# Kernel optimization log

Measured on AMD Instinct MI355X. Metric: run time of the kernel, lower is better.

The kernel has to match this reference:

```python
import jax, jax.numpy as jnp
import numpy as np

# SMPL kinematic tree (parents[0] is the root and unused in the loop)
PARENTS = (0, 0, 0, 0, 1, 2, 3, 4, 5, 6, 7, 8, 9, 9, 9, 12, 13, 14, 16, 17, 18, 19, 20, 21)
N_BATCH, N_VERTS, N_JOINTS, N_BETAS, N_POSE, N_COCO = 1024, 6890, 24, 10, 207, 19


def setup_inputs() -> dict:
    key = jax.random.key(0)
    ks = jax.random.split(key, 8)
    return {
        "beta": jax.random.normal(ks[0], (N_BATCH, N_BETAS), jnp.float32) * 0.5,
        "theta": jax.random.normal(ks[1], (N_BATCH, N_JOINTS * 3), jnp.float32) * 0.3,
        "v_template": jax.random.normal(ks[2], (N_VERTS, 3), jnp.float32),
        "shapedirs": jax.random.normal(ks[3], (N_BETAS, N_VERTS * 3), jnp.float32) * 0.01,
        "J_regressor": jax.random.uniform(ks[4], (N_VERTS, N_JOINTS), jnp.float32) / N_VERTS,
        "posedirs": jax.random.normal(ks[5], (N_POSE, N_VERTS * 3), jnp.float32) * 0.01,
        "weights": jax.random.uniform(ks[6], (N_VERTS, N_JOINTS), jnp.float32),
        "joint_regressor": jax.random.uniform(ks[7], (N_VERTS, N_COCO), jnp.float32) / N_VERTS,
    }


def batch_rodrigues(theta):
    """theta: (M, 3) axis-angle -> (M, 3, 3) rotation matrices."""
    angle = jnp.sqrt(jnp.sum(theta * theta, axis=-1, keepdims=True) + 1e-8)  # (M,1)
    r = theta / angle
    c = jnp.cos(angle)[..., None]  # (M,1,1)
    s = jnp.sin(angle)[..., None]
    rx, ry, rz = r[:, 0], r[:, 1], r[:, 2]
    z = jnp.zeros_like(rx)
    K = jnp.stack([z, -rz, ry, rz, z, -rx, -ry, rx, z], axis=-1).reshape(-1, 3, 3)
    outer = r[:, :, None] * r[:, None, :]
    eye = jnp.eye(3, dtype=theta.dtype)
    return c * eye + s * K + (1.0 - c) * outer


def global_rigid_transform(Rs, J):
    """Rs: (N,24,3,3), J: (N,24,3) -> (J_transformed (N,24,3), A (N,24,4,4))."""
    N = Rs.shape[0]
    bot = jnp.broadcast_to(jnp.array([0.0, 0.0, 0.0, 1.0], Rs.dtype), (N, 1, 4))

    def make_A(R, t):  # R: (N,3,3), t: (N,3)
        top = jnp.concatenate([R, t[:, :, None]], axis=2)  # (N,3,4)
        return jnp.concatenate([top, bot], axis=1)  # (N,4,4)

    results = [make_A(Rs[:, 0], J[:, 0])]
    for i in range(1, N_JOINTS):
        t_rel = J[:, i] - J[:, PARENTS[i]]
        results.append(jnp.matmul(results[PARENTS[i]], make_A(Rs[:, i], t_rel)))
    res = jnp.stack(results, axis=1)  # (N,24,4,4)
    J_transformed = res[:, :, :3, 3]
    # A = res - pack(res @ [J; 0]) : subtract rotated rest joints from translation column
    J_homo = jnp.concatenate([J, jnp.zeros((N, N_JOINTS, 1), Rs.dtype)], axis=2)  # (N,24,4)
    init_bone = jnp.einsum('njab,njb->nja', res, J_homo)  # (N,24,4)
    A = res - jnp.concatenate([jnp.zeros((N, N_JOINTS, 4, 3), Rs.dtype), init_bone[..., None]], axis=-1)
    return J_transformed, A


def reference(beta, theta, v_template, shapedirs, J_regressor, posedirs, weights, joint_regressor):
    N = beta.shape[0]
    # shape blend: (N,10) @ (10, V*3) -> (N,V,3)
    v_shaped = (beta @ shapedirs).reshape(N, N_VERTS, 3) + v_template
    # rest-pose joints: (N,V,3) x (V,24) -> (N,24,3)
    J = jnp.einsum('nva,vj->nja', v_shaped, J_regressor)
    # pose rotations
    Rs = batch_rodrigues(theta.reshape(-1, 3)).reshape(N, N_JOINTS, 3, 3)
    # pose blend: (N,207) @ (207, V*3)
    pose_feature = (Rs[:, 1:] - jnp.eye(3, dtype=Rs.dtype)).reshape(N, N_POSE)
    v_posed = (pose_feature @ posedirs).reshape(N, N_VERTS, 3) + v_shaped
    # kinematic chain
    _, A = global_rigid_transform(Rs, J)
    # LBS: per-vertex 4x4 transform
    T = jnp.einsum('vj,njab->nvab', weights, A)  # (N,V,4,4)
    v_homo = jnp.concatenate([v_posed, jnp.ones((N, N_VERTS, 1), v_posed.dtype)], axis=2)
    verts = jnp.einsum('nvab,nvb->nva', T, v_homo)[:, :, :3]  # (N,V,3)
    joints = jnp.einsum('nva,vj->nja', verts, joint_regressor)  # (N,19,3)
    return joints
```

## Files before the change

kernel.cpp:

```cpp
#include <hip/hip_runtime.h>

#define NB 1024
#define NV 6890
#define VP 6912
#define NJ 24
#define NBETA 10
#define NPOSE 207
#define NK 19
#define NKJ 456
#define NCOL 1368
#define KR 218
#define AR 219
#define VSTR 20670
#define RTP 16
#define NVC 216
#define CFP 32
#define KSPLIT 12
#define KSTEPS 18

typedef __attribute__((ext_vector_type(8))) short bf16x8;
typedef __attribute__((ext_vector_type(4))) float f32x4;

#define AP_PLANE ((size_t)3*RTP*NVC*64*8)
#define BP_PLANE ((size_t)CFP*NVC*64*8)
#define USH_TOTAL (2*AP_PLANE + 2*BP_PLANE)
#define SZ_OUT   ((size_t)AR*NCOL)
#define SZ_COEF  ((size_t)KR*NB)
#define SZ_AW    ((size_t)NB*288)
#define SZ_JS    (11ull*24*3)
#define SZ_M     ((size_t)NB*NCOL)

__device__ inline void bf_split(float x, unsigned short& h, unsigned short& l) {
    unsigned u = __float_as_uint(x);
    h = (unsigned short)(u >> 16);
    float hf = __uint_as_float((unsigned)h << 16);
    float lf = x - hf;
    l = (unsigned short)(__float_as_uint(lf) >> 16);
}

__global__ __launch_bounds__(256) void k_at2(const float* __restrict__ pd,
                                             const float* __restrict__ sd,
                                             const float* __restrict__ vt,
                                             unsigned short* __restrict__ APH,
                                             unsigned short* __restrict__ APL) {
    int tid = threadIdx.x;
    int u = blockIdx.x * 4 + (tid >> 6);
    int rt = u / NVC, vc = u - rt * NVC;
    int rl = tid & 15, lh = (tid >> 4) & 3;
    int r = rt * 16 + rl;
    int v0 = (vc * 4 + lh) * 8;

    float f[24];
    if (r >= AR) {
#pragma unroll
        for (int i = 0; i < 24; i++) f[i] = 0.f;
    } else if (r == 218) {
#pragma unroll
        for (int i = 0; i < 24; i++) f[i] = (v0 + i / 3 < NV) ? 1.0f : 0.f;
    } else {
        const float* src = (r < NPOSE) ? (pd + (size_t)r * VSTR)
                         : (r < 217)   ? (sd + (size_t)(r - NPOSE) * VSTR)
                                       : vt;
        if (v0 + 8 <= NV) {
            const float2* p = (const float2*)(src + 3 * v0);
#pragma unroll
            for (int q = 0; q < 12; q++) {
                float2 t = p[q];
                f[2 * q] = t.x; f[2 * q + 1] = t.y;
            }
        } else {
#pragma unroll
            for (int i = 0; i < 24; i++)
                f[i] = (v0 + i / 3 < NV) ? src[3 * v0 + i] : 0.f;
        }
    }

    int lane = lh * 16 + rl;
#pragma unroll
    for (int a = 0; a < 3; a++) {
        union { unsigned short u16[8]; int4 v4; } H, L;
#pragma unroll
        for (int e = 0; e < 8; e++) bf_split(f[3 * e + a], H.u16[e], L.u16[e]);
        size_t off = (((size_t)(a * RTP + rt) * NVC + vc) * 64 + lane) * 8;
        *(int4*)&APH[off] = H.v4;
        *(int4*)&APL[off] = L.v4;
    }
}

__global__ __launch_bounds__(256) void k_cw2(const float* __restrict__ jr,
                                             const float* __restrict__ w,
                                             unsigned short* __restrict__ BPH,
                                             unsigned short* __restrict__ BPL) {
    int tid = threadIdx.x;
    int u = blockIdx.x * 4 + (tid >> 6);
    int cf = u / NVC, vc = u - cf * NVC;
    int cl = tid & 15, lh = (tid >> 4) & 3;
    int col = cf * 16 + cl;
    int v0 = (vc * 4 + lh) * 8;
    int k = col / NJ, j = col - k * NJ;
    bool okc = (col < NKJ);

    union { unsigned short u16[8]; int4 v4; } H, L;
#pragma unroll
    for (int e = 0; e < 8; e++) {
        int v = v0 + e;
        float val = (okc && v < NV) ? jr[v * NK + k] * w[v * NJ + j] : 0.f;
        bf_split(val, H.u16[e], L.u16[e]);
    }
    size_t off = (((size_t)cf * NVC + vc) * 64 + (lh * 16 + cl)) * 8;
    *(int4*)&BPH[off] = H.v4;
    *(int4*)&BPL[off] = L.v4;
}

__global__ __launch_bounds__(256) void k_js2(const float* __restrict__ Jreg,
                                             const float* __restrict__ sd,
                                             const float* __restrict__ vt,
                                             float* __restrict__ JS) {
    int row = blockIdx.x % 11;
    int c   = blockIdx.x / 11;
    int tid = threadIdx.x;
    int lane = tid & 63;
    const float* src = (row < NBETA) ? (sd + (size_t)row * VSTR) : vt;

    float acc[72];
#pragma unroll
    for (int o = 0; o < 72; o++) acc[o] = 0.f;

    for (int iv = 0; iv < 4; ++iv) {
        int v = c * 1024 + iv * 256 + tid;
        float jrg[24];
        float s0 = 0.f, s1 = 0.f, s2 = 0.f;
        if (v < NV) {
#pragma unroll
            for (int q = 0; q < 6; q++) {
                float4 f = *(const float4*)&Jreg[v * NJ + q * 4];
                jrg[q * 4 + 0] = f.x; jrg[q * 4 + 1] = f.y;
                jrg[q * 4 + 2] = f.z; jrg[q * 4 + 3] = f.w;
            }
            s0 = src[3 * v]; s1 = src[3 * v + 1]; s2 = src[3 * v + 2];
        } else {
#pragma unroll
            for (int q = 0; q < 24; q++) jrg[q] = 0.f;
        }
#pragma unroll
        for (int j = 0; j < 24; j++) {
            acc[j * 3 + 0] += jrg[j] * s0;
            acc[j * 3 + 1] += jrg[j] * s1;
            acc[j * 3 + 2] += jrg[j] * s2;
        }
    }
#pragma unroll
    for (int o = 0; o < 72; o++) {
#pragma unroll
        for (int off = 1; off < 64; off <<= 1)
            acc[o] += __shfl_xor(acc[o], off);
    }
    if (lane == 0) {
#pragma unroll
        for (int o = 0; o < 72; o++) atomicAdd(&JS[row * 72 + o], acc[o]);
    }
}

__global__ __launch_bounds__(64) void k_pose(const float* __restrict__ beta,
                                             const float* __restrict__ theta,
                                             const float* __restrict__ JS,
                                             float* __restrict__ coefT,
                                             float* __restrict__ Aw) {
    int n = blockIdx.x;
    int tid = threadIdx.x;
    __shared__ float Rs[24][9];
    __shared__ float Jl[24][3];
    __shared__ float G[24][12];

    if (tid < NJ) {
        int j = tid;
        float x = theta[n * 72 + j * 3 + 0];
        float y = theta[n * 72 + j * 3 + 1];
        float z = theta[n * 72 + j * 3 + 2];
        float ang = sqrtf(x * x + y * y + z * z + 1e-8f);
        float inv = 1.0f / ang;
        float rx = x * inv, ry = y * inv, rz = z * inv;
        float ct = cosf(ang), st = sinf(ang), oc = 1.0f - ct;
        float R[9];
        R[0] = ct + oc * rx * rx;  R[1] = -st * rz + oc * rx * ry; R[2] =  st * ry + oc * rx * rz;
        R[3] =  st * rz + oc * ry * rx; R[4] = ct + oc * ry * ry;  R[5] = -st * rx + oc * ry * rz;
        R[6] = -st * ry + oc * rz * rx; R[7] =  st * rx + oc * rz * ry; R[8] = ct + oc * rz * rz;
#pragma unroll
        for (int e = 0; e < 9; e++) Rs[j][e] = R[e];
        if (j >= 1) {
#pragma unroll
            for (int e = 0; e < 9; e++)
                coefT[(size_t)((j - 1) * 9 + e) * NB + n] =
                    R[e] - ((e == 0 || e == 4 || e == 8) ? 1.0f : 0.0f);
        }
    }
    if (tid < NBETA) coefT[(size_t)(NPOSE + tid) * NB + n] = beta[n * NBETA + tid];
    if (tid == 63)   coefT[(size_t)217 * NB + n] = 1.0f;
    __syncthreads();

    for (int idx = tid; idx < 72; idx += 64) {
        int j = idx / 3, a = idx - j * 3;
        float acc = JS[(NBETA * NJ + j) * 3 + a];
#pragma unroll
        for (int b = 0; b < NBETA; b++) acc += beta[n * NBETA + b] * JS[(b * NJ + j) * 3 + a];
        Jl[j][a] = acc;
    }
    __syncthreads();

    if (tid < 12) {
        int r = tid >> 2, cc = tid & 3;
        G[0][tid] = (cc < 3) ? Rs[0][r * 3 + cc] : Jl[0][r];
    }
    __syncthreads();

    const int PAR[24] = {0,0,0,0,1,2,3,4,5,6,7,8,9,9,9,12,13,14,16,17,18,19,20,21};
#pragma unroll
    for (int i = 1; i < NJ; i++) {
        int p = PAR[i];
        if (tid < 12) {
            int r = tid >> 2, cc = tid & 3;
            float g0 = G[p][r * 4 + 0], g1 = G[p][r * 4 + 1];
            float g2 = G[p][r * 4 + 2], g3 = G[p][r * 4 + 3];
            float val;
            if (cc < 3) {
                val = g0 * Rs[i][cc] + g1 * Rs[i][3 + cc] + g2 * Rs[i][6 + cc];
            } else {
                float t0 = Jl[i][0] - Jl[p][0];
                float t1 = Jl[i][1] - Jl[p][1];
                float t2 = Jl[i][2] - Jl[p][2];
                val = g0 * t0 + g1 * t1 + g2 * t2 + g3;
            }
            G[i][tid] = val;
        }
        __syncthreads();
    }

    for (int idx = tid; idx < 288; idx += 64) {
        int j = idx / 12, e = idx - j * 12;
        float val;
        if (e < 9) {
            int r = e / 3, cc = e - 3 * (e / 3);
            val = G[j][r * 4 + cc];
        } else {
            int r = e - 9;
            val = G[j][r * 4 + 3] -
                  (G[j][r * 4 + 0] * Jl[j][0] + G[j][r * 4 + 1] * Jl[j][1] +
                   G[j][r * 4 + 2] * Jl[j][2]);
        }
        Aw[(size_t)n * 288 + idx] = val;
    }
}

__global__ __launch_bounds__(256) void k_gemmP(const unsigned short* __restrict__ APH,
                                               const unsigned short* __restrict__ APL,
                                               const unsigned short* __restrict__ BPH,
                                               const unsigned short* __restrict__ BPL,
                                               float* __restrict__ OUTB) {
    int bid = blockIdx.x;
    int logical = (bid & 7) * 72 + (bid >> 3);
    int ks = logical / 48;
    int rem = logical - ks * 48;
    int a  = rem >> 4;
    int mt = (rem >> 3) & 1;
    int nt = rem & 7;

    int tid = threadIdx.x;
    int lane = tid & 63, wv = tid >> 6;
    int wm = wv >> 1, wn = wv & 1;
    int lr = lane & 15, lc = lane >> 4;

    int aBase = a * RTP + mt * 8;
    int nBase = nt * 4;

    __shared__ __align__(16) unsigned short stage[2][24 * 512];

#define STAGE(B, VC) do {                                                        \
    _Pragma("unroll")                                                            \
    for (int q = 0; q < 6; ++q) {                                                \
        int f = wv * 6 + q;                                                      \
        const unsigned short* g;                                                 \
        if (f < 16) {                                                            \
            int rt_l = f >> 1;                                                   \
            const unsigned short* pl = (f & 1) ? APL : APH;                      \
            g = pl + (((size_t)(aBase + rt_l) * NVC + (VC)) << 9) + lane * 8;    \
        } else {                                                                 \
            int cf_l = (f - 16) >> 1;                                            \
            const unsigned short* pl = (f & 1) ? BPL : BPH;                      \
            g = pl + (((size_t)(nBase + cf_l) * NVC + (VC)) << 9) + lane * 8;    \
        }                                                                        \
        __builtin_amdgcn_global_load_lds(                                        \
            (const __attribute__((address_space(1))) unsigned int*)g,            \
            (__attribute__((address_space(3))) unsigned int*)&stage[B][f * 512], \
            16, 0, 0);                                                           \
    }                                                                            \
} while (0)

    f32x4 acc[4][2] = {};
    int vc0 = ks * KSTEPS;

    STAGE(0, vc0);
    __syncthreads();

    int cur = 0;
    for (int t = 0; t < KSTEPS; ++t) {
        if (t + 1 < KSTEPS) STAGE(cur ^ 1, vc0 + t + 1);

        bf16x8 aH[4], aL[4], bH[2], bL[2];
#pragma unroll
        for (int mi = 0; mi < 4; mi++) {
            int rt_l = wm * 4 + mi;
            aH[mi] = *(const bf16x8*)&stage[cur][(2 * rt_l) * 512 + lane * 8];
            aL[mi] = *(const bf16x8*)&stage[cur][(2 * rt_l + 1) * 512 + lane * 8];
        }
#pragma unroll
        for (int ni = 0; ni < 2; ni++) {
            int cf_l = wn * 2 + ni;
            bH[ni] = *(const bf16x8*)&stage[cur][(16 + 2 * cf_l) * 512 + lane * 8];
            bL[ni] = *(const bf16x8*)&stage[cur][(16 + 2 * cf_l + 1) * 512 + lane * 8];
        }
#pragma unroll
        for (int mi = 0; mi < 4; mi++)
#pragma unroll
            for (int ni = 0; ni < 2; ni++) {
                acc[mi][ni] = __builtin_amdgcn_mfma_f32_16x16x32_bf16(aH[mi], bH[ni], acc[mi][ni], 0, 0, 0);
                acc[mi][ni] = __builtin_amdgcn_mfma_f32_16x16x32_bf16(aH[mi], bL[ni], acc[mi][ni], 0, 0, 0);
                acc[mi][ni] = __builtin_amdgcn_mfma_f32_16x16x32_bf16(aL[mi], bH[ni], acc[mi][ni], 0, 0, 0);
            }
        __syncthreads();
        cur ^= 1;
    }

#pragma unroll
    for (int mi = 0; mi < 4; mi++) {
        int r0 = mt * 128 + wm * 64 + mi * 16 + lc * 4;
        if (r0 >= AR) continue;
#pragma unroll
        for (int ni = 0; ni < 2; ni++) {
            int c = nt * 64 + wn * 32 + ni * 16 + lr;
            if (c >= NKJ) continue;
#pragma unroll
            for (int q = 0; q < 4; ++q) {
                int r = r0 + q;
                if (r < AR)
                    atomicAdd(&OUTB[(size_t)r * NCOL + a * NKJ + c], acc[mi][ni][q]);
            }
        }
    }
}

__global__ __launch_bounds__(256) void k_gemmM(const float* __restrict__ coefT,
                                               const float* __restrict__ OUTB,
                                               float* __restrict__ M) {
    int bid = blockIdx.x;
    int mt = bid & 31, nt = bid >> 5;
    int mb = mt * 32, nb = nt * 64;
    __shared__ float Cs[2][32][32];
    __shared__ float Bs[2][32][64];
    int tid = threadIdx.x;
    int tm = tid & 15, tn = tid >> 4;

    float rc[4], rb[8];
#define LOADM(T) do {                                                    \
    int _kb = (T) * 32;                                                  \
    _Pragma("unroll") for (int p = 0; p < 4; p++) {                      \
        int idx = tid + p * 256;                                         \
        int kk = idx >> 5, nl = idx & 31;                                \
        int r = _kb + kk;                                                \
        rc[p] = (r < KR) ? coefT[(size_t)r * NB + mb + nl] : 0.f; }      \
    _Pragma("unroll") for (int p = 0; p < 8; p++) {                      \
        int idx = tid + p * 256;                                         \
        int kk = idx >> 6, m = idx & 63;                                 \
        int r = _kb + kk;                                                \
        int col = nb + m;                                                \
        rb[p] = (r < KR && col < NCOL) ? OUTB[(size_t)r * NCOL + col] : 0.f; } \
} while (0)

    LOADM(0);
    float acc[2][4] = {};
    int cur = 0;
    for (int t = 0; t < 7; ++t) {
#pragma unroll
        for (int p = 0; p < 4; p++) {
            int idx = tid + p * 256;
            Cs[cur][idx >> 5][idx & 31] = rc[p];
        }
#pragma unroll
        for (int p = 0; p < 8; p++) {
            int idx = tid + p * 256;
            Bs[cur][idx >> 6][idx & 63] = rb[p];
        }
        __syncthreads();
        if (t < 6) LOADM(t + 1);
#pragma unroll
        for (int kk = 0; kk < 32; kk++) {
            float2 cv = *(const float2*)&Cs[cur][kk][tm * 2];
            float4 bv = *(const float4*)&Bs[cur][kk][tn * 4];
            float cm[2] = {cv.x, cv.y};
            float bn[4] = {bv.x, bv.y, bv.z, bv.w};
#pragma unroll
            for (int i = 0; i < 2; i++)
#pragma unroll
                for (int j = 0; j < 4; j++) acc[i][j] += cm[i] * bn[j];
        }
        __syncthreads();
        cur ^= 1;
    }
#pragma unroll
    for (int i = 0; i < 2; i++) {
        int n = mb + tm * 2 + i;
#pragma unroll
        for (int j = 0; j < 4; j++) {
            int col = nb + tn * 4 + j;
            if (col < NCOL) M[(size_t)n * NCOL + col] = acc[i][j];
        }
    }
}

__global__ void k_joints(const float* __restrict__ M, const float* __restrict__ Aw,
                         const float* __restrict__ OUTB, float* __restrict__ out) {
    int idx = blockIdx.x * 256 + threadIdx.x;
    if (idx >= NB * NK * 3) return;
    int n = idx / (NK * 3);
    int rem = idx - n * (NK * 3);
    int k = rem / 3, a = rem - k * 3;
    const float* A = Aw + (size_t)n * 288;
    const float* Mn = M + (size_t)n * NCOL;
    float o = 0.f;
#pragma unroll
    for (int j = 0; j < NJ; j++) {
        int kj = k * NJ + j;
        const float* Aj = A + j * 12;
        o += Aj[a * 3 + 0] * Mn[kj]
           + Aj[a * 3 + 1] * Mn[NKJ + kj]
           + Aj[a * 3 + 2] * Mn[2 * NKJ + kj]
           + OUTB[(size_t)218 * NCOL + kj] * Aj[9 + a];
    }
    out[idx] = o;
}

extern "C" void kernel_launch(void* const* d_in, const int* in_sizes, int n_in,
                              void* d_out, int out_size, void* d_ws, size_t ws_size,
                              hipStream_t stream) {
    const float* beta  = (const float*)d_in[0];
    const float* theta = (const float*)d_in[1];
    const float* vt    = (const float*)d_in[2];
    const float* sd    = (const float*)d_in[3];
    const float* Jreg  = (const float*)d_in[4];
    const float* pd    = (const float*)d_in[5];
    const float* w     = (const float*)d_in[6];
    const float* jr    = (const float*)d_in[7];

    unsigned short* ush = (unsigned short*)d_ws;
    unsigned short* APH = ush;
    unsigned short* APL = APH + AP_PLANE;
    unsigned short* BPH = APL + AP_PLANE;
    unsigned short* BPL = BPH + BP_PLANE;
    float* fbase = (float*)(ush + USH_TOTAL);
    float* OUTB  = fbase;
    float* coefT = OUTB + SZ_OUT;
    float* Aw    = coefT + SZ_COEF;
    float* JS    = Aw + SZ_AW;
    float* M     = JS + SZ_JS;
    float* out   = (float*)d_out;

    hipMemsetAsync(OUTB, 0, (SZ_OUT + SZ_COEF + SZ_AW + SZ_JS) * sizeof(float), stream);
    k_at2<<<16 * NVC / 4, 256, 0, stream>>>(pd, sd, vt, APH, APL);
    k_cw2<<<CFP * NVC / 4, 256, 0, stream>>>(jr, w, BPH, BPL);
    k_js2<<<11 * 7, 256, 0, stream>>>(Jreg, sd, vt, JS);
    k_pose<<<NB, 64, 0, stream>>>(beta, theta, JS, coefT, Aw);
    k_gemmP<<<2 * 8 * 3 * KSPLIT, 256, 0, stream>>>(APH, APL, BPH, BPL, OUTB);
    k_gemmM<<<32 * 22, 256, 0, stream>>>(coefT, OUTB, M);
    k_joints<<<(NB * NK * 3 + 255) / 256, 256, 0, stream>>>(M, Aw, OUTB, out);
}
```

Measured before the change: 186.9 us.

## Move second GEMM to split-bf16 MFMA and merge prep kernels into one launch

The fp32 SIMT GEMM that forms M (coefT times OUTB) is replaced by a packing kernel that splits both operands into bf16 high/low fragment planes, followed by an MFMA GEMM using three bf16 products per tile to approximate fp32 accuracy. The three weight-preprocessing kernels are fused into one launch selected by block index. The memset is shrunk to the buffers that actually accumulate atomically. This trades an extra pack pass and workspace for matrix-core throughput and fewer launches, with a small precision risk from the split-bf16 scheme.

```diff
diff --git a/kernel.cpp b/kernel.cpp
--- a/kernel.cpp
+++ b/kernel.cpp
@@ -17,17 +17,22 @@
 #define CFP 32
 #define KSPLIT 12
 #define KSTEPS 18
+#define NF2 64
+#define KF2 7
+#define CF2 88
 
 typedef __attribute__((ext_vector_type(8))) short bf16x8;
 typedef __attribute__((ext_vector_type(4))) float f32x4;
 
 #define AP_PLANE ((size_t)3*RTP*NVC*64*8)
 #define BP_PLANE ((size_t)CFP*NVC*64*8)
-#define USH_TOTAL (2*AP_PLANE + 2*BP_PLANE)
+#define CP_PLANE ((size_t)NF2*KF2*64*8)
+#define OP_PLANE ((size_t)CF2*KF2*64*8)
+#define USH_TOTAL (2*AP_PLANE + 2*BP_PLANE + 2*CP_PLANE + 2*OP_PLANE)
 #define SZ_OUT   ((size_t)AR*NCOL)
+#define SZ_JS    (11ull*24*3)
 #define SZ_COEF  ((size_t)KR*NB)
 #define SZ_AW    ((size_t)NB*288)
-#define SZ_JS    (11ull*24*3)
 #define SZ_M     ((size_t)NB*NCOL)
 
 __device__ inline void bf_split(float x, unsigned short& h, unsigned short& l) {
@@ -38,126 +43,123 @@
     l = (unsigned short)(__float_as_uint(lf) >> 16);
 }
 
-__global__ __launch_bounds__(256) void k_at2(const float* __restrict__ pd,
-                                             const float* __restrict__ sd,
-                                             const float* __restrict__ vt,
-                                             unsigned short* __restrict__ APH,
-                                             unsigned short* __restrict__ APL) {
+#define PREP_AT 864
+#define PREP_CW 1728
+#define PREP_JS 77
+
+__global__ __launch_bounds__(256) void k_prep(const float* __restrict__ pd,
+                                              const float* __restrict__ sd,
+                                              const float* __restrict__ vt,
+                                              const float* __restrict__ jr,
+                                              const float* __restrict__ w,
+                                              const float* __restrict__ Jreg,
+                                              unsigned short* __restrict__ APH,
+                                              unsigned short* __restrict__ APL,
+                                              unsigned short* __restrict__ BPH,
+                                              unsigned short* __restrict__ BPL,
+                                              float* __restrict__ JS) {
+    int bx = blockIdx.x;
     int tid = threadIdx.x;
-    int u = blockIdx.x * 4 + (tid >> 6);
-    int rt = u / NVC, vc = u - rt * NVC;
-    int rl = tid & 15, lh = (tid >> 4) & 3;
-    int r = rt * 16 + rl;
-    int v0 = (vc * 4 + lh) * 8;
-
-    float f[24];
-    if (r >= AR) {
-#pragma unroll
-        for (int i = 0; i < 24; i++) f[i] = 0.f;
-    } else if (r == 218) {
-#pragma unroll
-        for (int i = 0; i < 24; i++) f[i] = (v0 + i / 3 < NV) ? 1.0f : 0.f;
+    if (bx < PREP_AT) {
+        int u = bx * 4 + (tid >> 6);
+        int rt = u / NVC, vc = u - rt * NVC;
+        int rl = tid & 15, lh = (tid >> 4) & 3;
+        int r = rt * 16 + rl;
+        int v0 = (vc * 4 + lh) * 8;
+        float f[24];
+        if (r >= AR) {
+#pragma unroll
+            for (int i = 0; i < 24; i++) f[i] = 0.f;
+        } else if (r == 218) {
+#pragma unroll
+            for (int i = 0; i < 24; i++) f[i] = (v0 + i / 3 < NV) ? 1.0f : 0.f;
+        } else {
+            const float* src = (r < NPOSE) ? (pd + (size_t)r * VSTR)
+                             : (r < 217)   ? (sd + (size_t)(r - NPOSE) * VSTR)
+                                           : vt;
+            if (v0 + 8 <= NV) {
+                const float2* p = (const float2*)(src + 3 * v0);
+#pragma unroll
+                for (int q = 0; q < 12; q++) {
+                    float2 t = p[q];
+                    f[2 * q] = t.x; f[2 * q + 1] = t.y;
+                }
+            } else {
+#pragma unroll
+                for (int i = 0; i < 24; i++)
+                    f[i] = (v0 + i / 3 < NV) ? src[3 * v0 + i] : 0.f;
+            }
+        }
+        int lane = lh * 16 + rl;
+#pragma unroll
+        for (int a = 0; a < 3; a++) {
+            union { unsigned short u16[8]; int4 v4; } H, L;
+#pragma unroll
+            for (int e = 0; e < 8; e++) bf_split(f[3 * e + a], H.u16[e], L.u16[e]);
+            size_t off = (((size_t)(a * RTP + rt) * NVC + vc) * 64 + lane) * 8;
+            *(int4*)&APH[off] = H.v4;
+            *(int4*)&APL[off] = L.v4;
+        }
+    } else if (bx < PREP_AT + PREP_CW) {
+        int u = (bx - PREP_AT) * 4 + (tid >> 6);
+        int cf = u / NVC, vc = u - cf * NVC;
+        int cl = tid & 15, lh = (tid >> 4) & 3;
+        int col = cf * 16 + cl;
+        int v0 = (vc * 4 + lh) * 8;
+        int k = col / NJ, j = col - k * NJ;
+        bool okc = (col < NKJ);
+        union { unsigned short u16[8]; int4 v4; } H, L;
+#pragma unroll
+        for (int e = 0; e < 8; e++) {
+            int v = v0 + e;
+            float val = (okc && v < NV) ? jr[v * NK + k] * w[v * NJ + j] : 0.f;
+            bf_split(val, H.u16[e], L.u16[e]);
+        }
+        size_t off = (((size_t)cf * NVC + vc) * 64 + (lh * 16 + cl)) * 8;
+        *(int4*)&BPH[off] = H.v4;
+        *(int4*)&BPL[off] = L.v4;
     } else {
-        const float* src = (r < NPOSE) ? (pd + (size_t)r * VSTR)
-                         : (r < 217)   ? (sd + (size_t)(r - NPOSE) * VSTR)
-                                       : vt;
-        if (v0 + 8 <= NV) {
-            const float2* p = (const float2*)(src + 3 * v0);
-#pragma unroll
-            for (int q = 0; q < 12; q++) {
-                float2 t = p[q];
-                f[2 * q] = t.x; f[2 * q + 1] = t.y;
-            }
-        } else {
-#pragma unroll
-            for (int i = 0; i < 24; i++)
-                f[i] = (v0 + i / 3 < NV) ? src[3 * v0 + i] : 0.f;
-        }
-    }
-
-    int lane = lh * 16 + rl;
-#pragma unroll
-    for (int a = 0; a < 3; a++) {
-        union { unsigned short u16[8]; int4 v4; } H, L;
-#pragma unroll
-        for (int e = 0; e < 8; e++) bf_split(f[3 * e + a], H.u16[e], L.u16[e]);
-        size_t off = (((size_t)(a * RTP + rt) * NVC + vc) * 64 + lane) * 8;
-        *(int4*)&APH[off] = H.v4;
-        *(int4*)&APL[off] = L.v4;
-    }
-}
-
-__global__ __launch_bounds__(256) void k_cw2(const float* __restrict__ jr,
-                                             const float* __restrict__ w,
-                                             unsigned short* __restrict__ BPH,
-                                             unsigned short* __restrict__ BPL) {
-    int tid = threadIdx.x;
-    int u = blockIdx.x * 4 + (tid >> 6);
-    int cf = u / NVC, vc = u - cf * NVC;
-    int cl = tid & 15, lh = (tid >> 4) & 3;
-    int col = cf * 16 + cl;
-    int v0 = (vc * 4 + lh) * 8;
-    int k = col / NJ, j = col - k * NJ;
-    bool okc = (col < NKJ);
-
-    union { unsigned short u16[8]; int4 v4; } H, L;
-#pragma unroll
-    for (int e = 0; e < 8; e++) {
-        int v = v0 + e;
-        float val = (okc && v < NV) ? jr[v * NK + k] * w[v * NJ + j] : 0.f;
-        bf_split(val, H.u16[e], L.u16[e]);
-    }
-    size_t off = (((size_t)cf * NVC + vc) * 64 + (lh * 16 + cl)) * 8;
-    *(int4*)&BPH[off] = H.v4;
-    *(int4*)&BPL[off] = L.v4;
-}
-
-__global__ __launch_bounds__(256) void k_js2(const float* __restrict__ Jreg,
-                                             const float* __restrict__ sd,
-                                             const float* __restrict__ vt,
-                                             float* __restrict__ JS) {
-    int row = blockIdx.x % 11;
-    int c   = blockIdx.x / 11;
-    int tid = threadIdx.x;
-    int lane = tid & 63;
-    const float* src = (row < NBETA) ? (sd + (size_t)row * VSTR) : vt;
-
-    float acc[72];
-#pragma unroll
-    for (int o = 0; o < 72; o++) acc[o] = 0.f;
-
-    for (int iv = 0; iv < 4; ++iv) {
-        int v = c * 1024 + iv * 256 + tid;
-        float jrg[24];
-        float s0 = 0.f, s1 = 0.f, s2 = 0.f;
-        if (v < NV) {
-#pragma unroll
-            for (int q = 0; q < 6; q++) {
-                float4 f = *(const float4*)&Jreg[v * NJ + q * 4];
-                jrg[q * 4 + 0] = f.x; jrg[q * 4 + 1] = f.y;
-                jrg[q * 4 + 2] = f.z; jrg[q * 4 + 3] = f.w;
-            }
-            s0 = src[3 * v]; s1 = src[3 * v + 1]; s2 = src[3 * v + 2];
-        } else {
-#pragma unroll
-            for (int q = 0; q < 24; q++) jrg[q] = 0.f;
-        }
-#pragma unroll
-        for (int j = 0; j < 24; j++) {
-            acc[j * 3 + 0] += jrg[j] * s0;
-            acc[j * 3 + 1] += jrg[j] * s1;
-            acc[j * 3 + 2] += jrg[j] * s2;
-        }
-    }
-#pragma unroll
-    for (int o = 0; o < 72; o++) {
-#pragma unroll
-        for (int off = 1; off < 64; off <<= 1)
-            acc[o] += __shfl_xor(acc[o], off);
-    }
-    if (lane == 0) {
-#pragma unroll
-        for (int o = 0; o < 72; o++) atomicAdd(&JS[row * 72 + o], acc[o]);
+        int b2 = bx - PREP_AT - PREP_CW;
+        int row = b2 % 11;
+        int c   = b2 / 11;
+        int lane = tid & 63;
+        const float* src = (row < NBETA) ? (sd + (size_t)row * VSTR) : vt;
+        float acc[72];
+#pragma unroll
+        for (int o = 0; o < 72; o++) acc[o] = 0.f;
+        for (int iv = 0; iv < 4; ++iv) {
+            int v = c * 1024 + iv * 256 + tid;
+            float jrg[24];
+            float s0 = 0.f, s1 = 0.f, s2 = 0.f;
+            if (v < NV) {
+#pragma unroll
+                for (int q = 0; q < 6; q++) {
+                    float4 f4 = *(const float4*)&Jreg[v * NJ + q * 4];
+                    jrg[q * 4 + 0] = f4.x; jrg[q * 4 + 1] = f4.y;
+                    jrg[q * 4 + 2] = f4.z; jrg[q * 4 + 3] = f4.w;
+                }
+                s0 = src[3 * v]; s1 = src[3 * v + 1]; s2 = src[3 * v + 2];
+            } else {
+#pragma unroll
+                for (int q = 0; q < 24; q++) jrg[q] = 0.f;
+            }
+#pragma unroll
+            for (int j = 0; j < 24; j++) {
+                acc[j * 3 + 0] += jrg[j] * s0;
+                acc[j * 3 + 1] += jrg[j] * s1;
+                acc[j * 3 + 2] += jrg[j] * s2;
+            }
+        }
+#pragma unroll
+        for (int o = 0; o < 72; o++) {
+#pragma unroll
+            for (int off = 1; off < 64; off <<= 1)
+                acc[o] += __shfl_xor(acc[o], off);
+        }
+        if (lane == 0) {
+#pragma unroll
+            for (int o = 0; o < 72; o++) atomicAdd(&JS[row * 72 + o], acc[o]);
+        }
     }
 }
 
@@ -348,70 +350,98 @@
     }
 }
 
-__global__ __launch_bounds__(256) void k_gemmM(const float* __restrict__ coefT,
-                                               const float* __restrict__ OUTB,
-                                               float* __restrict__ M) {
+__global__ __launch_bounds__(256) void k_pack(const float* __restrict__ coefT,
+                                              const float* __restrict__ OUTB,
+                                              unsigned short* __restrict__ CPH,
+                                              unsigned short* __restrict__ CPL,
+                                              unsigned short* __restrict__ OPH,
+                                              unsigned short* __restrict__ OPL) {
+    int gid = blockIdx.x * 256 + threadIdx.x;
+    if (blockIdx.x < 112) {
+        int idx = gid;
+        int lane = idx & 63;
+        int t = idx >> 6;
+        int kf = t % KF2, nf = t / KF2;
+        int n = nf * 16 + (lane & 15);
+        int rbase = kf * 32 + (lane >> 4) * 8;
+        union { unsigned short u16[8]; int4 v4; } H, L;
+#pragma unroll
+        for (int e = 0; e < 8; e++) {
+            int r = rbase + e;
+            float val = (r < KR) ? coefT[(size_t)r * NB + n] : 0.f;
+            bf_split(val, H.u16[e], L.u16[e]);
+        }
+        *(int4*)&CPH[(size_t)idx * 8] = H.v4;
+        *(int4*)&CPL[(size_t)idx * 8] = L.v4;
+    } else {
+        int idx = gid - 112 * 256;
+        int lane = idx & 63;
+        int t = idx >> 6;
+        int kf = t % KF2, cf = t / KF2;
+        int col = cf * 16 + (lane & 15);
+        int rbase = kf * 32 + (lane >> 4) * 8;
+        union { unsigned short u16[8]; int4 v4; } H, L;
+#pragma unroll
+        for (int e = 0; e < 8; e++) {
+            int r = rbase + e;
+            float val = (r < KR && col < NCOL) ? OUTB[(size_t)r * NCOL + col] : 0.f;
+            bf_split(val, H.u16[e], L.u16[e]);
+        }
+        *(int4*)&OPH[(size_t)idx * 8] = H.v4;
+        *(int4*)&OPL[(size_t)idx * 8] = L.v4;
+    }
+}
+
+__global__ __launch_bounds__(256) void k_gemmM2(const unsigned short* __restrict__ CPH,
+                                                const unsigned short* __restrict__ CPL,
+                                                const unsigned short* __restrict__ OPH,
+                                                const unsigned short* __restrict__ OPL,
+                                                float* __restrict__ M) {
     int bid = blockIdx.x;
-    int mt = bid & 31, nt = bid >> 5;
-    int mb = mt * 32, nb = nt * 64;
-    __shared__ float Cs[2][32][32];
-    __shared__ float Bs[2][32][64];
+    int mtile = bid & 15, ctile = bid >> 4;
     int tid = threadIdx.x;
-    int tm = tid & 15, tn = tid >> 4;
-
-    float rc[4], rb[8];
-#define LOADM(T) do {                                                    \
-    int _kb = (T) * 32;                                                  \
-    _Pragma("unroll") for (int p = 0; p < 4; p++) {                      \
-        int idx = tid + p * 256;                                         \
-        int kk = idx >> 5, nl = idx & 31;                                \
-        int r = _kb + kk;                                                \
-        rc[p] = (r < KR) ? coefT[(size_t)r * NB + mb + nl] : 0.f; }      \
-    _Pragma("unroll") for (int p = 0; p < 8; p++) {                      \
-        int idx = tid + p * 256;                                         \
-        int kk = idx >> 6, m = idx & 63;                                 \
-        int r = _kb + kk;                                                \
-        int col = nb + m;                                                \
-        rb[p] = (r < KR && col < NCOL) ? OUTB[(size_t)r * NCOL + col] : 0.f; } \
-} while (0)
-
-    LOADM(0);
-    float acc[2][4] = {};
-    int cur = 0;
-    for (int t = 0; t < 7; ++t) {
-#pragma unroll
-        for (int p = 0; p < 4; p++) {
-            int idx = tid + p * 256;
-            Cs[cur][idx >> 5][idx & 31] = rc[p];
-        }
-#pragma unroll
-        for (int p = 0; p < 8; p++) {
-            int idx = tid + p * 256;
-            Bs[cur][idx >> 6][idx & 63] = rb[p];
-        }
-        __syncthreads();
-        if (t < 6) LOADM(t + 1);
-#pragma unroll
-        for (int kk = 0; kk < 32; kk++) {
-            float2 cv = *(const float2*)&Cs[cur][kk][tm * 2];
-            float4 bv = *(const float4*)&Bs[cur][kk][tn * 4];
-            float cm[2] = {cv.x, cv.y};
-            float bn[4] = {bv.x, bv.y, bv.z, bv.w};
-#pragma unroll
-            for (int i = 0; i < 2; i++)
-#pragma unroll
-                for (int j = 0; j < 4; j++) acc[i][j] += cm[i] * bn[j];
-        }
-        __syncthreads();
-        cur ^= 1;
-    }
-#pragma unroll
-    for (int i = 0; i < 2; i++) {
-        int n = mb + tm * 2 + i;
-#pragma unroll
-        for (int j = 0; j < 4; j++) {
-            int col = nb + tn * 4 + j;
-            if (col < NCOL) M[(size_t)n * NCOL + col] = acc[i][j];
+    int lane = tid & 63, wv = tid >> 6;
+    int wm = wv >> 1, wn = wv & 1;
+    int lr = lane & 15, lc = lane >> 4;
+
+    f32x4 acc[2][2] = {};
+#pragma unroll
+    for (int kf = 0; kf < KF2; ++kf) {
+        bf16x8 aH[2], aL[2], bH[2], bL[2];
+#pragma unroll
+        for (int mi = 0; mi < 2; mi++) {
+            int nf = mtile * 4 + wm * 2 + mi;
+            size_t off = ((size_t)(nf * KF2 + kf) * 64 + lane) * 8;
+            aH[mi] = *(const bf16x8*)(CPH + off);
+            aL[mi] = *(const bf16x8*)(CPL + off);
+        }
+#pragma unroll
+        for (int ni = 0; ni < 2; ni++) {
+            int cf = ctile * 4 + wn * 2 + ni;
+            size_t off = ((size_t)(cf * KF2 + kf) * 64 + lane) * 8;
+            bH[ni] = *(const bf16x8*)(OPH + off);
+            bL[ni] = *(const bf16x8*)(OPL + off);
+        }
+#pragma unroll
+        for (int mi = 0; mi < 2; mi++)
+#pragma unroll
+            for (int ni = 0; ni < 2; ni++) {
+                acc[mi][ni] = __builtin_amdgcn_mfma_f32_16x16x32_bf16(aH[mi], bH[ni], acc[mi][ni], 0, 0, 0);
+                acc[mi][ni] = __builtin_amdgcn_mfma_f32_16x16x32_bf16(aH[mi], bL[ni], acc[mi][ni], 0, 0, 0);
+                acc[mi][ni] = __builtin_amdgcn_mfma_f32_16x16x32_bf16(aL[mi], bH[ni], acc[mi][ni], 0, 0, 0);
+            }
+    }
+
+#pragma unroll
+    for (int mi = 0; mi < 2; mi++) {
+        int n0 = mtile * 64 + wm * 32 + mi * 16 + lc * 4;
+#pragma unroll
+        for (int ni = 0; ni < 2; ni++) {
+            int col = ctile * 64 + wn * 32 + ni * 16 + lr;
+            if (col >= NCOL) continue;
+#pragma unroll
+            for (int q = 0; q < 4; ++q)
+                M[(size_t)(n0 + q) * NCOL + col] = acc[mi][ni][q];
         }
     }
 }
@@ -455,20 +485,24 @@
     unsigned short* APL = APH + AP_PLANE;
     unsigned short* BPH = APL + AP_PLANE;
     unsigned short* BPL = BPH + BP_PLANE;
+    unsigned short* CPH = BPL + BP_PLANE;
+    unsigned short* CPL = CPH + CP_PLANE;
+    unsigned short* OPH = CPL + CP_PLANE;
+    unsigned short* OPL = OPH + OP_PLANE;
     float* fbase = (float*)(ush + USH_TOTAL);
     float* OUTB  = fbase;
-    float* coefT = OUTB + SZ_OUT;
+    float* JS    = OUTB + SZ_OUT;
+    float* coefT = JS + SZ_JS;
     float* Aw    = coefT + SZ_COEF;
-    float* JS    = Aw + SZ_AW;
-    float* M     = JS + SZ_JS;
+    float* M     = Aw + SZ_AW;
     float* out   = (float*)d_out;
 
-    hipMemsetAsync(OUTB, 0, (SZ_OUT + SZ_COEF + SZ_AW + SZ_JS) * sizeof(float), stream);
-    k_at2<<<16 * NVC / 4, 256, 0, stream>>>(pd, sd, vt, APH, APL);
-    k_cw2<<<CFP * NVC / 4, 256, 0, stream>>>(jr, w, BPH, BPL);
-    k_js2<<<11 * 7, 256, 0, stream>>>(Jreg, sd, vt, JS);
+    hipMemsetAsync(OUTB, 0, (SZ_OUT + SZ_JS) * sizeof(float), stream);
+    k_prep<<<PREP_AT + PREP_CW + PREP_JS, 256, 0, stream>>>(pd, sd, vt, jr, w, Jreg,
+                                                            APH, APL, BPH, BPL, JS);
     k_pose<<<NB, 64, 0, stream>>>(beta, theta, JS, coefT, Aw);
     k_gemmP<<<2 * 8 * 3 * KSPLIT, 256, 0, stream>>>(APH, APL, BPH, BPL, OUTB);
-    k_gemmM<<<32 * 22, 256, 0, stream>>>(coefT, OUTB, M);
+    k_pack<<<266, 256, 0, stream>>>(coefT, OUTB, CPH, CPL, OPH, OPL);
+    k_gemmM2<<<16 * 22, 256, 0, stream>>>(CPH, CPL, OPH, OPL, M);
     k_joints<<<(NB * NK * 3 + 255) / 256, 256, 0, stream>>>(M, Aw, OUTB, out);
 }
```

Result: faster. 172.4 us (-7.8%).
